# Kernel tuning notes

Hardware: AMD Instinct MI355X
Metric: run time of the kernel (lower is better)

## Reference

```python
import jax, jax.numpy as jnp
import numpy as np

NUM_ITERATIONS = 3


def _squash_elementwise(s):
    # Faithful to the source: squared_norm is summed over the trailing
    # singleton dim, so squash acts elementwise: x^2 * x / ((1+x^2) * |x|).
    sq = s * s
    return sq * s / ((1.0 + sq) * jnp.sqrt(sq))


def setup_inputs() -> dict:
    key = jax.random.key(0)
    k1, k2 = jax.random.split(key)
    B, R, J, O, I = 512, 1152, 10, 16, 8  # batch, num_routes, num_capsules, out_ch, in_ch
    x = jax.random.normal(k1, (B, R, I), dtype=jnp.float32)
    W = jax.random.normal(k2, (R, J, O, I), dtype=jnp.float32)
    return {"x": x, "W": W}


def reference(x, W):
    # u_hat[b,r,j,o] = W[r,j,o,:] @ x[b,r,:]   (the torch matmul over [O,I]x[I,1])
    u_hat = jnp.einsum('rjoi,bri->brjo', W, x)  # [B,R,J,O]
    R, J = W.shape[0], W.shape[1]
    b = jnp.zeros((R, J), dtype=u_hat.dtype)  # b_ij shared across batch
    v = None
    for it in range(NUM_ITERATIONS):
        c = jax.nn.softmax(b, axis=0)                 # softmax over routes (dim=1 in torch)
        s = jnp.einsum('rj,brjo->bjo', c, u_hat)      # weighted sum over routes
        v = _squash_elementwise(s)                    # [B,J,O]
        if it < NUM_ITERATIONS - 1:
            a = jnp.einsum('brjo,bjo->brj', u_hat, v)  # agreement
            b = b + a.mean(axis=0)                     # mean over batch, as in source
    # original returns v_j.squeeze(1) -> [B, num_capsules, out_channels, 1]
    return v[..., None]
```

## Files before the change

kernel.cpp:

```cpp
#include <hip/hip_runtime.h>


#define B_   512
#define R_   1152
#define JO_  160
#define K_   9216

typedef __attribute__((ext_vector_type(4))) float f32x4;
typedef __attribute__((ext_vector_type(8))) short bf16x8;

__device__ __forceinline__ short f2bf(float f) {
  unsigned int u = __float_as_uint(f);
  unsigned int r = (u + 0x7FFFu + ((u >> 16) & 1u)) >> 16;
  return (short)r;
}

__global__ __launch_bounds__(256) void init_kernel(float* __restrict__ bias,
                                                   float* __restrict__ c) {
  int idx = blockIdx.x * 256 + threadIdx.x;
  if (idx < R_ * 10) {
    bias[idx] = 0.0f;
    c[idx] = 1.0f / (float)R_;
  }
}

__global__ __launch_bounds__(256) void xafbuild_kernel(
    const float* __restrict__ x, short* __restrict__ xaf) {
  int gid = blockIdx.x * 256 + threadIdx.x;
  int lane = gid & 63, f = gid >> 6;
  int ks = f % 288, m16 = f / 288;
  int row = m16 * 16 + (lane & 15);
  int k0 = ks * 32 + (lane >> 4) * 8;
  const float4* p = (const float4*)(x + (size_t)row * K_ + k0);
  float4 a = p[0], b = p[1];
  bf16x8 pk;
  pk[0] = f2bf(a.x); pk[1] = f2bf(a.y); pk[2] = f2bf(a.z); pk[3] = f2bf(a.w);
  pk[4] = f2bf(b.x); pk[5] = f2bf(b.y); pk[6] = f2bf(b.z); pk[7] = f2bf(b.w);
  ((bf16x8*)xaf)[gid] = pk;
}

__global__ __launch_bounds__(256) void xtfbuild_kernel(
    const float* __restrict__ x, short* __restrict__ xtf) {
  int gid = blockIdx.x * 256 + threadIdx.x;
  int lane = gid & 63, f = gid >> 6;
  int kb = f & 15, rp = f >> 4;
  int b0 = kb * 32 + (lane >> 4) * 8;
  const float* p = x + (size_t)b0 * K_ + rp * 16 + (lane & 15);
  bf16x8 pk;
#pragma unroll
  for (int t = 0; t < 8; ++t) pk[t] = f2bf(p[(size_t)t * K_]);
  ((bf16x8*)xtf)[gid] = pk;
}

__global__ __launch_bounds__(256) void wcbuild_kernel(
    const float* __restrict__ W, const float* __restrict__ c,
    short* __restrict__ wcf) {
  int idx = blockIdx.x * 256 + threadIdx.x;
  int lane = idx & 63;
  int rest = idx >> 6;
  int nb = rest % 10, kb = rest / 10;
  int k0 = kb * 32 + (lane >> 4) * 8;
  int r = k0 >> 3;
  int j = nb, o = lane & 15;
  const float4* wp = (const float4*)(W + (((size_t)r * 10 + j) * 16 + o) * 8);
  float4 a = wp[0], b = wp[1];
  float cs = c[r * 10 + j];
  bf16x8 pk;
  pk[0] = f2bf(a.x * cs); pk[1] = f2bf(a.y * cs);
  pk[2] = f2bf(a.z * cs); pk[3] = f2bf(a.w * cs);
  pk[4] = f2bf(b.x * cs); pk[5] = f2bf(b.y * cs);
  pk[6] = f2bf(b.z * cs); pk[7] = f2bf(b.w * cs);
  ((bf16x8*)wcf)[idx] = pk;
}

__global__ __launch_bounds__(256) void sgemm_kernel(
    const float* __restrict__ x, const short* __restrict__ xaf,
    const short* __restrict__ wcf, float* __restrict__ part, int spk) {
  const int tid = threadIdx.x;
  const int w = tid >> 6, lane = tid & 63;
  const int m16 = blockIdx.x * 4 + w;
  const int ks0 = blockIdx.y * spk;

  f32x4 acc[10] = {};
  const bf16x8* bp = (const bf16x8*)wcf + ((size_t)ks0 * 640 + lane);
  if (xaf) {
    const bf16x8* ap = (const bf16x8*)xaf + ((size_t)m16 * 288 + ks0) * 64 + lane;
    for (int ks = 0; ks < spk; ++ks) {
      bf16x8 af = ap[0];
      ap += 64;
#pragma unroll
      for (int nb = 0; nb < 10; ++nb)
        acc[nb] = __builtin_amdgcn_mfma_f32_16x16x32_bf16(af, bp[nb * 64],
                                                          acc[nb], 0, 0, 0);
      bp += 640;
    }
  } else {
    const int row = m16 * 16 + (lane & 15);
    const float* xrow = x + (size_t)row * K_ + (lane >> 4) * 8;
    for (int ks = ks0; ks < ks0 + spk; ++ks) {
      const float4* ap = (const float4*)(xrow + ks * 32);
      float4 a0 = ap[0], a1 = ap[1];
      bf16x8 af;
      af[0] = f2bf(a0.x); af[1] = f2bf(a0.y); af[2] = f2bf(a0.z); af[3] = f2bf(a0.w);
      af[4] = f2bf(a1.x); af[5] = f2bf(a1.y); af[6] = f2bf(a1.z); af[7] = f2bf(a1.w);
#pragma unroll
      for (int nb = 0; nb < 10; ++nb)
        acc[nb] = __builtin_amdgcn_mfma_f32_16x16x32_bf16(af, bp[nb * 64],
                                                          acc[nb], 0, 0, 0);
      bp += 640;
    }
  }
  float* pp = part + (size_t)blockIdx.y * (B_ * JO_) +
              (size_t)(m16 * 16 + (lane >> 4) * 4) * JO_ + (lane & 15);
#pragma unroll
  for (int nb = 0; nb < 10; ++nb)
#pragma unroll
    for (int q = 0; q < 4; ++q)
      pp[q * JO_ + nb * 16] = acc[nb][q];
}

template <int KS>
__global__ __launch_bounds__(512) void squash_kernel(
    const float* __restrict__ part, short* __restrict__ vfrag,
    float* __restrict__ out) {
  __shared__ float vsm[32][17];
  const int tid = threadIdx.x;
  const int kb = blockIdx.x / 10, nb = blockIdx.x - (blockIdx.x / 10) * 10;
  const int bl = tid >> 4, col = tid & 15;
  const int b = kb * 32 + bl, jo = nb * 16 + col;
  const float* pe = part + (size_t)b * JO_ + jo;
  float pv[KS];
#pragma unroll
  for (int ks = 0; ks < KS; ++ks) pv[ks] = pe[(size_t)ks * (B_ * JO_)];
  float s = 0.0f;
#pragma unroll
  for (int ks = 0; ks < KS; ++ks) s += pv[ks];
  float val = s * fabsf(s) / (1.0f + s * s);
  if (out) out[(size_t)b * JO_ + jo] = val;
  if (vfrag) {
    vsm[bl][col] = val;
    __syncthreads();
    if (tid < 64) {
      bf16x8 pk;
#pragma unroll
      for (int t = 0; t < 8; ++t)
        pk[t] = f2bf(vsm[(tid >> 4) * 8 + t][tid & 15]);
      ((bf16x8*)vfrag)[(size_t)blockIdx.x * 64 + tid] = pk;
    }
  }
}

__global__ __launch_bounds__(256) void agree_kernel(
    const float* __restrict__ x, const short* __restrict__ xtf,
    const float* __restrict__ W, const short* __restrict__ vfrag,
    float* __restrict__ bias) {
  __shared__ float Msm[4][16][176];
  __shared__ float red[320];
  const int tid = threadIdx.x;
  const int w = tid >> 6, lane = tid & 63;
  const int rp = blockIdx.x;
  const int r0 = rp * 2;

  f32x4 acc[10] = {};
  if (xtf) {
    const bf16x8* ap = (const bf16x8*)xtf + ((size_t)rp * 16 + w * 4) * 64 + lane;
    const bf16x8* bp = (const bf16x8*)vfrag + ((size_t)(w * 4) * 640 + lane);
#pragma unroll
    for (int ks = 0; ks < 4; ++ks) {
      bf16x8 af = ap[0];
      ap += 64;
#pragma unroll
      for (int nb = 0; nb < 10; ++nb)
        acc[nb] = __builtin_amdgcn_mfma_f32_16x16x32_bf16(af, bp[nb * 64],
                                                          acc[nb], 0, 0, 0);
      bp += 640;
    }
  } else {
    const int rowa = lane & 15;
    const float* xp = x + (size_t)rp * 16 + rowa;
    for (int ks = 0; ks < 4; ++ks) {
      int b0 = w * 128 + ks * 32 + (lane >> 4) * 8;
      bf16x8 af;
#pragma unroll
      for (int t = 0; t < 8; ++t) af[t] = f2bf(xp[(size_t)(b0 + t) * K_]);
      const bf16x8* bp = (const bf16x8*)vfrag + ((w * 4 + ks) * 640 + lane);
#pragma unroll
      for (int nb = 0; nb < 10; ++nb)
        acc[nb] = __builtin_amdgcn_mfma_f32_16x16x32_bf16(af, bp[nb * 64],
                                                          acc[nb], 0, 0, 0);
    }
  }
  {
    int colc = lane & 15, rbase = (lane >> 4) * 4;
#pragma unroll
    for (int nb = 0; nb < 10; ++nb)
#pragma unroll
      for (int q = 0; q < 4; ++q)
        Msm[w][rbase + q][nb * 16 + colc] = acc[nb][q];
  }
  __syncthreads();
  for (int idx = tid; idx < 320; idx += 256) {
    int rr = idx / 160, jo = idx - rr * 160;
    int j = jo >> 4, o = jo & 15;
    float p = 0.0f;
    const float* wp = W + (((size_t)(r0 + rr) * 10 + j) * 16 + o) * 8;
#pragma unroll
    for (int i = 0; i < 8; ++i) {
      float m = Msm[0][rr * 8 + i][jo] + Msm[1][rr * 8 + i][jo] +
                Msm[2][rr * 8 + i][jo] + Msm[3][rr * 8 + i][jo];
      p += wp[i] * m;
    }
    red[idx] = p;
  }
  __syncthreads();
  if (tid < 20) {
    int rr = tid / 10, j = tid - rr * 10;
    float s = 0.0f;
#pragma unroll
    for (int o = 0; o < 16; ++o) s += red[rr * 160 + j * 16 + o];
    bias[(r0 + rr) * 10 + j] += s * (1.0f / 512.0f);
  }
}

__global__ __launch_bounds__(256) void softmax_kernel(
    const float* __restrict__ bias, float* __restrict__ c) {
  __shared__ float red[256];
  const int j = blockIdx.x;
  const int tid = threadIdx.x;
  float m = -1e30f;
  for (int r = tid; r < R_; r += 256) m = fmaxf(m, bias[r * 10 + j]);
  red[tid] = m;
  __syncthreads();
  for (int s = 128; s > 0; s >>= 1) {
    if (tid < s) red[tid] = fmaxf(red[tid], red[tid + s]);
    __syncthreads();
  }
  m = red[0];
  __syncthreads();
  float sum = 0.0f;
  for (int r = tid; r < R_; r += 256) sum += expf(bias[r * 10 + j] - m);
  red[tid] = sum;
  __syncthreads();
  for (int s = 128; s > 0; s >>= 1) {
    if (tid < s) red[tid] += red[tid + s];
    __syncthreads();
  }
  float inv = 1.0f / red[0];
  for (int r = tid; r < R_; r += 256)
    c[r * 10 + j] = expf(bias[r * 10 + j] - m) * inv;
}

extern "C" void kernel_launch(void* const* d_in, const int* in_sizes, int n_in,
                              void* d_out, int out_size, void* d_ws,
                              size_t ws_size, hipStream_t stream) {
  const float* x = (const float*)d_in[0];
  const float* W = (const float*)d_in[1];
  float* out = (float*)d_out;
  char* ws = (char*)d_ws;

  const size_t BASE = 3205120;
  const size_t PARTB = 327680;
  const size_t XAFB = 9437184, XTFB = 9437184;

  float* bias  = (float*)(ws);
  float* c     = (float*)(ws + 46080);
  short* wcf   = (short*)(ws + 92160);
  short* vfrag = (short*)(ws + 3041280);

  size_t avail = ws_size > BASE ? ws_size - BASE : 0;
  int KS = 1;
  bool useXaf = false, useXtf = false;
  if (avail >= 32 * PARTB + XAFB + XTFB) { KS = 32; useXaf = useXtf = true; }
  else if (avail >= 16 * PARTB + XAFB + XTFB) { KS = 16; useXaf = useXtf = true; }
  else if (avail >= 16 * PARTB + XAFB) { KS = 16; useXaf = true; }
  else if (avail >= 16 * PARTB) KS = 16;
  else if (avail >= 8 * PARTB) KS = 8;
  else if (avail >= 4 * PARTB) KS = 4;
  else if (avail >= 2 * PARTB) KS = 2;
  int spk = 288 / KS;

  size_t cur = BASE;
  short* xaf = nullptr;
  short* xtf = nullptr;
  if (useXaf) { xaf = (short*)(ws + cur); cur += XAFB; }
  if (useXtf) { xtf = (short*)(ws + cur); cur += XTFB; }
  float* part = (float*)(ws + cur);

  init_kernel<<<45, 256, 0, stream>>>(bias, c);
  if (useXaf) xafbuild_kernel<<<2304, 256, 0, stream>>>(x, xaf);
  if (useXtf) xtfbuild_kernel<<<2304, 256, 0, stream>>>(x, xtf);

  for (int it = 0; it < 3; ++it) {
    wcbuild_kernel<<<720, 256, 0, stream>>>(W, c, wcf);
    sgemm_kernel<<<dim3(8, KS), 256, 0, stream>>>(x, xaf, wcf, part, spk);
    short* vf = (it < 2) ? vfrag : nullptr;
    float* o = (it == 2) ? out : nullptr;
    switch (KS) {
      case 32: squash_kernel<32><<<160, 512, 0, stream>>>(part, vf, o); break;
      case 16: squash_kernel<16><<<160, 512, 0, stream>>>(part, vf, o); break;
      case 8:  squash_kernel<8><<<160, 512, 0, stream>>>(part, vf, o); break;
      case 4:  squash_kernel<4><<<160, 512, 0, stream>>>(part, vf, o); break;
      case 2:  squash_kernel<2><<<160, 512, 0, stream>>>(part, vf, o); break;
      default: squash_kernel<1><<<160, 512, 0, stream>>>(part, vf, o); break;
    }
    if (it < 2) {
      agree_kernel<<<576, 256, 0, stream>>>(x, xtf, W, vfrag, bias);
      softmax_kernel<<<10, 256, 0, stream>>>(bias, c);
    }
  }
}
```

Baseline: 98.31 us.

## Fuse split-K GEMM with squash via in-block LDS reduction

Replaces the split-K sgemm plus separate squash kernel with a single forward kernel that splits K across four wave groups inside one block and reduces their partials through shared memory before applying squash. This removes the global partial buffer and one launch per iteration. The first iteration applies the uniform 1/1152 coupling as a scalar instead of scaling W. The cost is far less parallelism: only 16 blocks each run a 72-step MFMA loop, where before the grid was 8 by up to 32 blocks.

```diff
diff --git a/kernel.cpp b/kernel.cpp
--- a/kernel.cpp
+++ b/kernel.cpp
@@ -15,13 +15,9 @@
   return (short)r;
 }
 
-__global__ __launch_bounds__(256) void init_kernel(float* __restrict__ bias,
-                                                   float* __restrict__ c) {
+__global__ __launch_bounds__(256) void init_kernel(float* __restrict__ bias) {
   int idx = blockIdx.x * 256 + threadIdx.x;
-  if (idx < R_ * 10) {
-    bias[idx] = 0.0f;
-    c[idx] = 1.0f / (float)R_;
-  }
+  if (idx < R_ * 10) bias[idx] = 0.0f;
 }
 
 __global__ __launch_bounds__(256) void xafbuild_kernel(
@@ -64,7 +60,7 @@
   int j = nb, o = lane & 15;
   const float4* wp = (const float4*)(W + (((size_t)r * 10 + j) * 16 + o) * 8);
   float4 a = wp[0], b = wp[1];
-  float cs = c[r * 10 + j];
+  float cs = c ? c[r * 10 + j] : 1.0f;
   bf16x8 pk;
   pk[0] = f2bf(a.x * cs); pk[1] = f2bf(a.y * cs);
   pk[2] = f2bf(a.z * cs); pk[3] = f2bf(a.w * cs);
@@ -73,19 +69,24 @@
   ((bf16x8*)wcf)[idx] = pk;
 }
 
-__global__ __launch_bounds__(256) void sgemm_kernel(
+template <bool SCALE>
+__global__ __launch_bounds__(512) void fwd_kernel(
     const float* __restrict__ x, const short* __restrict__ xaf,
-    const short* __restrict__ wcf, float* __restrict__ part, int spk) {
+    const short* __restrict__ wcf, short* __restrict__ vfrag,
+    float* __restrict__ out) {
+  __shared__ float sm[20992];
   const int tid = threadIdx.x;
   const int w = tid >> 6, lane = tid & 63;
-  const int m16 = blockIdx.x * 4 + w;
-  const int ks0 = blockIdx.y * spk;
+  const int mw = w & 1, kw = w >> 1;
+  const int bb = blockIdx.x;
+  const int m16 = bb * 2 + mw;
 
   f32x4 acc[10] = {};
-  const bf16x8* bp = (const bf16x8*)wcf + ((size_t)ks0 * 640 + lane);
+  const bf16x8* bp = (const bf16x8*)wcf + ((size_t)(kw * 72) * 640 + lane);
   if (xaf) {
-    const bf16x8* ap = (const bf16x8*)xaf + ((size_t)m16 * 288 + ks0) * 64 + lane;
-    for (int ks = 0; ks < spk; ++ks) {
+    const bf16x8* ap =
+        (const bf16x8*)xaf + ((size_t)m16 * 288 + kw * 72) * 64 + lane;
+    for (int st = 0; st < 72; ++st) {
       bf16x8 af = ap[0];
       ap += 64;
 #pragma unroll
@@ -95,14 +96,16 @@
       bp += 640;
     }
   } else {
-    const int row = m16 * 16 + (lane & 15);
+    const int row = bb * 32 + mw * 16 + (lane & 15);
     const float* xrow = x + (size_t)row * K_ + (lane >> 4) * 8;
-    for (int ks = ks0; ks < ks0 + spk; ++ks) {
-      const float4* ap = (const float4*)(xrow + ks * 32);
-      float4 a0 = ap[0], a1 = ap[1];
+    for (int st = 0; st < 72; ++st) {
+      const float4* apf = (const float4*)(xrow + (kw * 72 + st) * 32);
+      float4 a0 = apf[0], a1 = apf[1];
       bf16x8 af;
-      af[0] = f2bf(a0.x); af[1] = f2bf(a0.y); af[2] = f2bf(a0.z); af[3] = f2bf(a0.w);
-      af[4] = f2bf(a1.x); af[5] = f2bf(a1.y); af[6] = f2bf(a1.z); af[7] = f2bf(a1.w);
+      af[0] = f2bf(a0.x); af[1] = f2bf(a0.y);
+      af[2] = f2bf(a0.z); af[3] = f2bf(a0.w);
+      af[4] = f2bf(a1.x); af[5] = f2bf(a1.y);
+      af[6] = f2bf(a1.z); af[7] = f2bf(a1.w);
 #pragma unroll
       for (int nb = 0; nb < 10; ++nb)
         acc[nb] = __builtin_amdgcn_mfma_f32_16x16x32_bf16(af, bp[nb * 64],
@@ -110,42 +113,57 @@
       bp += 640;
     }
   }
-  float* pp = part + (size_t)blockIdx.y * (B_ * JO_) +
-              (size_t)(m16 * 16 + (lane >> 4) * 4) * JO_ + (lane & 15);
-#pragma unroll
-  for (int nb = 0; nb < 10; ++nb)
-#pragma unroll
-    for (int q = 0; q < 4; ++q)
-      pp[q * JO_ + nb * 16] = acc[nb][q];
-}
-
-template <int KS>
-__global__ __launch_bounds__(512) void squash_kernel(
-    const float* __restrict__ part, short* __restrict__ vfrag,
-    float* __restrict__ out) {
-  __shared__ float vsm[32][17];
-  const int tid = threadIdx.x;
-  const int kb = blockIdx.x / 10, nb = blockIdx.x - (blockIdx.x / 10) * 10;
-  const int bl = tid >> 4, col = tid & 15;
-  const int b = kb * 32 + bl, jo = nb * 16 + col;
-  const float* pe = part + (size_t)b * JO_ + jo;
-  float pv[KS];
-#pragma unroll
-  for (int ks = 0; ks < KS; ++ks) pv[ks] = pe[(size_t)ks * (B_ * JO_)];
-  float s = 0.0f;
-#pragma unroll
-  for (int ks = 0; ks < KS; ++ks) s += pv[ks];
-  float val = s * fabsf(s) / (1.0f + s * s);
-  if (out) out[(size_t)b * JO_ + jo] = val;
+  {
+    float* dst = sm + (size_t)(w * 64 + lane) * 41;
+#pragma unroll
+    for (int nb = 0; nb < 10; ++nb)
+#pragma unroll
+      for (int q = 0; q < 4; ++q) dst[nb * 4 + q] = acc[nb][q];
+  }
+  __syncthreads();
+  float vals[10];
+  const int e0 = tid * 10;
+  const int mwr = e0 / 2560;
+  const int rem = e0 - mwr * 2560;
+  const int lr = rem / 40, c0 = rem - lr * 40;
+#pragma unroll
+  for (int u = 0; u < 10; ++u) {
+    int cc = c0 + u;
+    float s = sm[((0 + mwr) * 64 + lr) * 41 + cc] +
+              sm[((2 + mwr) * 64 + lr) * 41 + cc] +
+              sm[((4 + mwr) * 64 + lr) * 41 + cc] +
+              sm[((6 + mwr) * 64 + lr) * 41 + cc];
+    if (SCALE) s *= (1.0f / 1152.0f);
+    vals[u] = s * fabsf(s) / (1.0f + s * s);
+  }
+  if (out) {
+#pragma unroll
+    for (int u = 0; u < 10; ++u) {
+      int cc = c0 + u;
+      int q = cc & 3, nb = cc >> 2;
+      int bl = mwr * 16 + (lr >> 4) * 4 + q;
+      int jo = nb * 16 + (lr & 15);
+      out[(size_t)(bb * 32 + bl) * JO_ + jo] = vals[u];
+    }
+  }
   if (vfrag) {
-    vsm[bl][col] = val;
     __syncthreads();
-    if (tid < 64) {
+#pragma unroll
+    for (int u = 0; u < 10; ++u) {
+      int cc = c0 + u;
+      int q = cc & 3, nb = cc >> 2;
+      int bl = mwr * 16 + (lr >> 4) * 4 + q;
+      int jo = nb * 16 + (lr & 15);
+      sm[bl * 162 + jo] = vals[u];
+    }
+    __syncthreads();
+    for (int ch = tid; ch < 640; ch += 512) {
+      int nb = ch >> 6, l2 = ch & 63;
       bf16x8 pk;
 #pragma unroll
       for (int t = 0; t < 8; ++t)
-        pk[t] = f2bf(vsm[(tid >> 4) * 8 + t][tid & 15]);
-      ((bf16x8*)vfrag)[(size_t)blockIdx.x * 64 + tid] = pk;
+        pk[t] = f2bf(sm[((l2 >> 4) * 8 + t) * 162 + nb * 16 + (l2 & 15)]);
+      ((bf16x8*)vfrag)[(size_t)(bb * 10 + nb) * 64 + l2] = pk;
     }
   }
 }
@@ -259,7 +277,6 @@
   char* ws = (char*)d_ws;
 
   const size_t BASE = 3205120;
-  const size_t PARTB = 327680;
   const size_t XAFB = 9437184, XTFB = 9437184;
 
   float* bias  = (float*)(ws);
@@ -267,42 +284,24 @@
   short* wcf   = (short*)(ws + 92160);
   short* vfrag = (short*)(ws + 3041280);
 
-  size_t avail = ws_size > BASE ? ws_size - BASE : 0;
-  int KS = 1;
-  bool useXaf = false, useXtf = false;
-  if (avail >= 32 * PARTB + XAFB + XTFB) { KS = 32; useXaf = useXtf = true; }
-  else if (avail >= 16 * PARTB + XAFB + XTFB) { KS = 16; useXaf = useXtf = true; }
-  else if (avail >= 16 * PARTB + XAFB) { KS = 16; useXaf = true; }
-  else if (avail >= 16 * PARTB) KS = 16;
-  else if (avail >= 8 * PARTB) KS = 8;
-  else if (avail >= 4 * PARTB) KS = 4;
-  else if (avail >= 2 * PARTB) KS = 2;
-  int spk = 288 / KS;
-
-  size_t cur = BASE;
   short* xaf = nullptr;
   short* xtf = nullptr;
-  if (useXaf) { xaf = (short*)(ws + cur); cur += XAFB; }
-  if (useXtf) { xtf = (short*)(ws + cur); cur += XTFB; }
-  float* part = (float*)(ws + cur);
-
-  init_kernel<<<45, 256, 0, stream>>>(bias, c);
-  if (useXaf) xafbuild_kernel<<<2304, 256, 0, stream>>>(x, xaf);
-  if (useXtf) xtfbuild_kernel<<<2304, 256, 0, stream>>>(x, xtf);
+  size_t cur = BASE;
+  if (ws_size >= cur + XAFB) { xaf = (short*)(ws + cur); cur += XAFB; }
+  if (ws_size >= cur + XTFB) { xtf = (short*)(ws + cur); cur += XTFB; }
+
+  init_kernel<<<45, 256, 0, stream>>>(bias);
+  if (xaf) xafbuild_kernel<<<2304, 256, 0, stream>>>(x, xaf);
+  if (xtf) xtfbuild_kernel<<<2304, 256, 0, stream>>>(x, xtf);
 
   for (int it = 0; it < 3; ++it) {
-    wcbuild_kernel<<<720, 256, 0, stream>>>(W, c, wcf);
-    sgemm_kernel<<<dim3(8, KS), 256, 0, stream>>>(x, xaf, wcf, part, spk);
+    wcbuild_kernel<<<720, 256, 0, stream>>>(W, (it == 0) ? nullptr : c, wcf);
     short* vf = (it < 2) ? vfrag : nullptr;
     float* o = (it == 2) ? out : nullptr;
-    switch (KS) {
-      case 32: squash_kernel<32><<<160, 512, 0, stream>>>(part, vf, o); break;
-      case 16: squash_kernel<16><<<160, 512, 0, stream>>>(part, vf, o); break;
-      case 8:  squash_kernel<8><<<160, 512, 0, stream>>>(part, vf, o); break;
-      case 4:  squash_kernel<4><<<160, 512, 0, stream>>>(part, vf, o); break;
-      case 2:  squash_kernel<2><<<160, 512, 0, stream>>>(part, vf, o); break;
-      default: squash_kernel<1><<<160, 512, 0, stream>>>(part, vf, o); break;
-    }
+    if (it == 0)
+      fwd_kernel<true><<<16, 512, 0, stream>>>(x, xaf, wcf, vf, o);
+    else
+      fwd_kernel<false><<<16, 512, 0, stream>>>(x, xaf, wcf, vf, o);
     if (it < 2) {
       agree_kernel<<<576, 256, 0, stream>>>(x, xtf, W, vfrag, bias);
       softmax_kernel<<<10, 256, 0, stream>>>(bias, c);
```

Result: slower. 367.4 us (+273.8%).

## Fuse coupling-weight construction into sgemm via LDS and drop init/softmax passes

Applied to the files above, without the earlier changes.

Removes the separate wcbuild and softmax kernels. Each sgemm block now builds its bf16 W*c tile directly in shared memory, computing c from bias plus per-capsule max and inverse-sum produced by a small stat kernel. The first iteration uses a uniform scale applied at the epilogue, and bias zeroing is folded into xafbuild. The workspace-dependent fallback paths are dropped, so the kernel now assumes a large workspace with KS fixed at 32. Each block recomputes 5760 W fragments and exps into 92KB of LDS, which may limit occupancy and duplicates W reads across the 8 x-blocks.

```diff
diff --git a/kernel.cpp b/kernel.cpp
--- a/kernel.cpp
+++ b/kernel.cpp
@@ -5,6 +5,8 @@
 #define R_   1152
 #define JO_  160
 #define K_   9216
+#define KS_  32
+#define SPK_ 9
 
 typedef __attribute__((ext_vector_type(4))) float f32x4;
 typedef __attribute__((ext_vector_type(8))) short bf16x8;
@@ -15,18 +17,11 @@
   return (short)r;
 }
 
-__global__ __launch_bounds__(256) void init_kernel(float* __restrict__ bias,
-                                                   float* __restrict__ c) {
-  int idx = blockIdx.x * 256 + threadIdx.x;
-  if (idx < R_ * 10) {
-    bias[idx] = 0.0f;
-    c[idx] = 1.0f / (float)R_;
-  }
-}
-
 __global__ __launch_bounds__(256) void xafbuild_kernel(
-    const float* __restrict__ x, short* __restrict__ xaf) {
+    const float* __restrict__ x, short* __restrict__ xaf,
+    float* __restrict__ bias) {
   int gid = blockIdx.x * 256 + threadIdx.x;
+  if (gid < R_ * 10) bias[gid] = 0.0f;
   int lane = gid & 63, f = gid >> 6;
   int ks = f % 288, m16 = f / 288;
   int row = m16 * 16 + (lane & 15);
@@ -52,74 +47,91 @@
   ((bf16x8*)xtf)[gid] = pk;
 }
 
-__global__ __launch_bounds__(256) void wcbuild_kernel(
-    const float* __restrict__ W, const float* __restrict__ c,
-    short* __restrict__ wcf) {
-  int idx = blockIdx.x * 256 + threadIdx.x;
-  int lane = idx & 63;
-  int rest = idx >> 6;
-  int nb = rest % 10, kb = rest / 10;
-  int k0 = kb * 32 + (lane >> 4) * 8;
-  int r = k0 >> 3;
-  int j = nb, o = lane & 15;
-  const float4* wp = (const float4*)(W + (((size_t)r * 10 + j) * 16 + o) * 8);
-  float4 a = wp[0], b = wp[1];
-  float cs = c[r * 10 + j];
-  bf16x8 pk;
-  pk[0] = f2bf(a.x * cs); pk[1] = f2bf(a.y * cs);
-  pk[2] = f2bf(a.z * cs); pk[3] = f2bf(a.w * cs);
-  pk[4] = f2bf(b.x * cs); pk[5] = f2bf(b.y * cs);
-  pk[6] = f2bf(b.z * cs); pk[7] = f2bf(b.w * cs);
-  ((bf16x8*)wcf)[idx] = pk;
-}
-
+__global__ __launch_bounds__(256) void stat_kernel(
+    const float* __restrict__ bias, float* __restrict__ mz) {
+  __shared__ float red[256];
+  const int j = blockIdx.x;
+  const int tid = threadIdx.x;
+  float m = -1e30f;
+  for (int r = tid; r < R_; r += 256) m = fmaxf(m, bias[r * 10 + j]);
+  red[tid] = m;
+  __syncthreads();
+  for (int s = 128; s > 0; s >>= 1) {
+    if (tid < s) red[tid] = fmaxf(red[tid], red[tid + s]);
+    __syncthreads();
+  }
+  m = red[0];
+  __syncthreads();
+  float sum = 0.0f;
+  for (int r = tid; r < R_; r += 256) sum += expf(bias[r * 10 + j] - m);
+  red[tid] = sum;
+  __syncthreads();
+  for (int s = 128; s > 0; s >>= 1) {
+    if (tid < s) red[tid] += red[tid + s];
+    __syncthreads();
+  }
+  if (tid == 0) {
+    mz[j] = m;
+    mz[10 + j] = 1.0f / red[0];
+  }
+}
+
+template <bool NEEDC>
 __global__ __launch_bounds__(256) void sgemm_kernel(
-    const float* __restrict__ x, const short* __restrict__ xaf,
-    const short* __restrict__ wcf, float* __restrict__ part, int spk) {
+    const short* __restrict__ xaf, const float* __restrict__ W,
+    const float* __restrict__ bias, const float* __restrict__ mz,
+    float* __restrict__ part) {
+  __shared__ short wls[5760 * 8];
   const int tid = threadIdx.x;
   const int w = tid >> 6, lane = tid & 63;
+  const int ks0 = blockIdx.y * SPK_;
+  bf16x8* wls8 = (bf16x8*)wls;
+
+  for (int q = 0; q < 23; ++q) {
+    int idx = q * 256 + tid;
+    if (idx < 5760) {
+      int l = idx & 63, sn = idx >> 6;
+      int nb = sn % 10, st = sn / 10;
+      int r = (ks0 + st) * 4 + (l >> 4);
+      int o = l & 15;
+      const float4* wp =
+          (const float4*)(W + (((size_t)r * 10 + nb) * 16 + o) * 8);
+      float4 a = wp[0], b = wp[1];
+      float cs = 1.0f;
+      if (NEEDC) cs = expf(bias[r * 10 + nb] - mz[nb]) * mz[10 + nb];
+      bf16x8 pk;
+      pk[0] = f2bf(a.x * cs); pk[1] = f2bf(a.y * cs);
+      pk[2] = f2bf(a.z * cs); pk[3] = f2bf(a.w * cs);
+      pk[4] = f2bf(b.x * cs); pk[5] = f2bf(b.y * cs);
+      pk[6] = f2bf(b.z * cs); pk[7] = f2bf(b.w * cs);
+      wls8[idx] = pk;
+    }
+  }
+  __syncthreads();
+
   const int m16 = blockIdx.x * 4 + w;
-  const int ks0 = blockIdx.y * spk;
-
   f32x4 acc[10] = {};
-  const bf16x8* bp = (const bf16x8*)wcf + ((size_t)ks0 * 640 + lane);
-  if (xaf) {
-    const bf16x8* ap = (const bf16x8*)xaf + ((size_t)m16 * 288 + ks0) * 64 + lane;
-    for (int ks = 0; ks < spk; ++ks) {
-      bf16x8 af = ap[0];
-      ap += 64;
-#pragma unroll
-      for (int nb = 0; nb < 10; ++nb)
-        acc[nb] = __builtin_amdgcn_mfma_f32_16x16x32_bf16(af, bp[nb * 64],
-                                                          acc[nb], 0, 0, 0);
-      bp += 640;
-    }
-  } else {
-    const int row = m16 * 16 + (lane & 15);
-    const float* xrow = x + (size_t)row * K_ + (lane >> 4) * 8;
-    for (int ks = ks0; ks < ks0 + spk; ++ks) {
-      const float4* ap = (const float4*)(xrow + ks * 32);
-      float4 a0 = ap[0], a1 = ap[1];
-      bf16x8 af;
-      af[0] = f2bf(a0.x); af[1] = f2bf(a0.y); af[2] = f2bf(a0.z); af[3] = f2bf(a0.w);
-      af[4] = f2bf(a1.x); af[5] = f2bf(a1.y); af[6] = f2bf(a1.z); af[7] = f2bf(a1.w);
-#pragma unroll
-      for (int nb = 0; nb < 10; ++nb)
-        acc[nb] = __builtin_amdgcn_mfma_f32_16x16x32_bf16(af, bp[nb * 64],
-                                                          acc[nb], 0, 0, 0);
-      bp += 640;
-    }
-  }
+  const bf16x8* ap = (const bf16x8*)xaf + ((size_t)m16 * 288 + ks0) * 64 + lane;
+  const bf16x8* lp = wls8 + lane;
+  for (int st = 0; st < SPK_; ++st) {
+    bf16x8 af = ap[0];
+    ap += 64;
+#pragma unroll
+    for (int nb = 0; nb < 10; ++nb)
+      acc[nb] = __builtin_amdgcn_mfma_f32_16x16x32_bf16(af, lp[nb * 64],
+                                                        acc[nb], 0, 0, 0);
+    lp += 640;
+  }
+  const float scale = NEEDC ? 1.0f : (1.0f / 1152.0f);
   float* pp = part + (size_t)blockIdx.y * (B_ * JO_) +
               (size_t)(m16 * 16 + (lane >> 4) * 4) * JO_ + (lane & 15);
 #pragma unroll
   for (int nb = 0; nb < 10; ++nb)
 #pragma unroll
     for (int q = 0; q < 4; ++q)
-      pp[q * JO_ + nb * 16] = acc[nb][q];
-}
-
-template <int KS>
+      pp[q * JO_ + nb * 16] = acc[nb][q] * scale;
+}
+
 __global__ __launch_bounds__(512) void squash_kernel(
     const float* __restrict__ part, short* __restrict__ vfrag,
     float* __restrict__ out) {
@@ -129,12 +141,12 @@
   const int bl = tid >> 4, col = tid & 15;
   const int b = kb * 32 + bl, jo = nb * 16 + col;
   const float* pe = part + (size_t)b * JO_ + jo;
-  float pv[KS];
-#pragma unroll
-  for (int ks = 0; ks < KS; ++ks) pv[ks] = pe[(size_t)ks * (B_ * JO_)];
+  float pv[KS_];
+#pragma unroll
+  for (int ks = 0; ks < KS_; ++ks) pv[ks] = pe[(size_t)ks * (B_ * JO_)];
   float s = 0.0f;
 #pragma unroll
-  for (int ks = 0; ks < KS; ++ks) s += pv[ks];
+  for (int ks = 0; ks < KS_; ++ks) s += pv[ks];
   float val = s * fabsf(s) / (1.0f + s * s);
   if (out) out[(size_t)b * JO_ + jo] = val;
   if (vfrag) {
@@ -151,9 +163,8 @@
 }
 
 __global__ __launch_bounds__(256) void agree_kernel(
-    const float* __restrict__ x, const short* __restrict__ xtf,
-    const float* __restrict__ W, const short* __restrict__ vfrag,
-    float* __restrict__ bias) {
+    const short* __restrict__ xtf, const float* __restrict__ W,
+    const short* __restrict__ vfrag, float* __restrict__ bias) {
   __shared__ float Msm[4][16][176];
   __shared__ float red[320];
   const int tid = threadIdx.x;
@@ -162,33 +173,17 @@
   const int r0 = rp * 2;
 
   f32x4 acc[10] = {};
-  if (xtf) {
-    const bf16x8* ap = (const bf16x8*)xtf + ((size_t)rp * 16 + w * 4) * 64 + lane;
-    const bf16x8* bp = (const bf16x8*)vfrag + ((size_t)(w * 4) * 640 + lane);
-#pragma unroll
-    for (int ks = 0; ks < 4; ++ks) {
-      bf16x8 af = ap[0];
-      ap += 64;
-#pragma unroll
-      for (int nb = 0; nb < 10; ++nb)
-        acc[nb] = __builtin_amdgcn_mfma_f32_16x16x32_bf16(af, bp[nb * 64],
-                                                          acc[nb], 0, 0, 0);
-      bp += 640;
-    }
-  } else {
-    const int rowa = lane & 15;
-    const float* xp = x + (size_t)rp * 16 + rowa;
-    for (int ks = 0; ks < 4; ++ks) {
-      int b0 = w * 128 + ks * 32 + (lane >> 4) * 8;
-      bf16x8 af;
-#pragma unroll
-      for (int t = 0; t < 8; ++t) af[t] = f2bf(xp[(size_t)(b0 + t) * K_]);
-      const bf16x8* bp = (const bf16x8*)vfrag + ((w * 4 + ks) * 640 + lane);
-#pragma unroll
-      for (int nb = 0; nb < 10; ++nb)
-        acc[nb] = __builtin_amdgcn_mfma_f32_16x16x32_bf16(af, bp[nb * 64],
-                                                          acc[nb], 0, 0, 0);
-    }
+  const bf16x8* ap = (const bf16x8*)xtf + ((size_t)rp * 16 + w * 4) * 64 + lane;
+  const bf16x8* bp = (const bf16x8*)vfrag + ((size_t)(w * 4) * 640 + lane);
+#pragma unroll
+  for (int ks = 0; ks < 4; ++ks) {
+    bf16x8 af = ap[0];
+    ap += 64;
+#pragma unroll
+    for (int nb = 0; nb < 10; ++nb)
+      acc[nb] = __builtin_amdgcn_mfma_f32_16x16x32_bf16(af, bp[nb * 64],
+                                                        acc[nb], 0, 0, 0);
+    bp += 640;
   }
   {
     int colc = lane & 15, rbase = (lane >> 4) * 4;
@@ -220,34 +215,6 @@
     for (int o = 0; o < 16; ++o) s += red[rr * 160 + j * 16 + o];
     bias[(r0 + rr) * 10 + j] += s * (1.0f / 512.0f);
   }
-}
-
-__global__ __launch_bounds__(256) void softmax_kernel(
-    const float* __restrict__ bias, float* __restrict__ c) {
-  __shared__ float red[256];
-  const int j = blockIdx.x;
-  const int tid = threadIdx.x;
-  float m = -1e30f;
-  for (int r = tid; r < R_; r += 256) m = fmaxf(m, bias[r * 10 + j]);
-  red[tid] = m;
-  __syncthreads();
-  for (int s = 128; s > 0; s >>= 1) {
-    if (tid < s) red[tid] = fmaxf(red[tid], red[tid + s]);
-    __syncthreads();
-  }
-  m = red[0];
-  __syncthreads();
-  float sum = 0.0f;
-  for (int r = tid; r < R_; r += 256) sum += expf(bias[r * 10 + j] - m);
-  red[tid] = sum;
-  __syncthreads();
-  for (int s = 128; s > 0; s >>= 1) {
-    if (tid < s) red[tid] += red[tid + s];
-    __syncthreads();
-  }
-  float inv = 1.0f / red[0];
-  for (int r = tid; r < R_; r += 256)
-    c[r * 10 + j] = expf(bias[r * 10 + j] - m) * inv;
 }
 
 extern "C" void kernel_launch(void* const* d_in, const int* in_sizes, int n_in,
@@ -258,54 +225,25 @@
   float* out = (float*)d_out;
   char* ws = (char*)d_ws;
 
-  const size_t BASE = 3205120;
-  const size_t PARTB = 327680;
-  const size_t XAFB = 9437184, XTFB = 9437184;
-
   float* bias  = (float*)(ws);
-  float* c     = (float*)(ws + 46080);
-  short* wcf   = (short*)(ws + 92160);
-  short* vfrag = (short*)(ws + 3041280);
-
-  size_t avail = ws_size > BASE ? ws_size - BASE : 0;
-  int KS = 1;
-  bool useXaf = false, useXtf = false;
-  if (avail >= 32 * PARTB + XAFB + XTFB) { KS = 32; useXaf = useXtf = true; }
-  else if (avail >= 16 * PARTB + XAFB + XTFB) { KS = 16; useXaf = useXtf = true; }
-  else if (avail >= 16 * PARTB + XAFB) { KS = 16; useXaf = true; }
-  else if (avail >= 16 * PARTB) KS = 16;
-  else if (avail >= 8 * PARTB) KS = 8;
-  else if (avail >= 4 * PARTB) KS = 4;
-  else if (avail >= 2 * PARTB) KS = 2;
-  int spk = 288 / KS;
-
-  size_t cur = BASE;
-  short* xaf = nullptr;
-  short* xtf = nullptr;
-  if (useXaf) { xaf = (short*)(ws + cur); cur += XAFB; }
-  if (useXtf) { xtf = (short*)(ws + cur); cur += XTFB; }
-  float* part = (float*)(ws + cur);
-
-  init_kernel<<<45, 256, 0, stream>>>(bias, c);
-  if (useXaf) xafbuild_kernel<<<2304, 256, 0, stream>>>(x, xaf);
-  if (useXtf) xtfbuild_kernel<<<2304, 256, 0, stream>>>(x, xtf);
-
-  for (int it = 0; it < 3; ++it) {
-    wcbuild_kernel<<<720, 256, 0, stream>>>(W, c, wcf);
-    sgemm_kernel<<<dim3(8, KS), 256, 0, stream>>>(x, xaf, wcf, part, spk);
-    short* vf = (it < 2) ? vfrag : nullptr;
-    float* o = (it == 2) ? out : nullptr;
-    switch (KS) {
-      case 32: squash_kernel<32><<<160, 512, 0, stream>>>(part, vf, o); break;
-      case 16: squash_kernel<16><<<160, 512, 0, stream>>>(part, vf, o); break;
-      case 8:  squash_kernel<8><<<160, 512, 0, stream>>>(part, vf, o); break;
-      case 4:  squash_kernel<4><<<160, 512, 0, stream>>>(part, vf, o); break;
-      case 2:  squash_kernel<2><<<160, 512, 0, stream>>>(part, vf, o); break;
-      default: squash_kernel<1><<<160, 512, 0, stream>>>(part, vf, o); break;
-    }
-    if (it < 2) {
-      agree_kernel<<<576, 256, 0, stream>>>(x, xtf, W, vfrag, bias);
-      softmax_kernel<<<10, 256, 0, stream>>>(bias, c);
-    }
-  }
-}
+  float* mz    = (float*)(ws + 46080);
+  short* vfrag = (short*)(ws + 46160);
+  short* xaf   = (short*)(ws + 210000);
+  short* xtf   = (short*)(ws + 9647184);
+  float* part  = (float*)(ws + 19084368);
+
+  xafbuild_kernel<<<2304, 256, 0, stream>>>(x, xaf, bias);
+  xtfbuild_kernel<<<2304, 256, 0, stream>>>(x, xtf);
+
+  sgemm_kernel<false><<<dim3(8, KS_), 256, 0, stream>>>(xaf, W, nullptr,
+                                                        nullptr, part);
+  squash_kernel<<<160, 512, 0, stream>>>(part, vfrag, nullptr);
+  agree_kernel<<<576, 256, 0, stream>>>(xtf, W, vfrag, bias);
+  stat_kernel<<<10, 256, 0, stream>>>(bias, mz);
+  sgemm_kernel<true><<<dim3(8, KS_), 256, 0, stream>>>(xaf, W, bias, mz, part);
+  squash_kernel<<<160, 512, 0, stream>>>(part, vfrag, nullptr);
+  agree_kernel<<<576, 256, 0, stream>>>(xtf, W, vfrag, bias);
+  stat_kernel<<<10, 256, 0, stream>>>(bias, mz);
+  sgemm_kernel<true><<<dim3(8, KS_), 256, 0, stream>>>(xaf, W, bias, mz, part);
+  squash_kernel<<<160, 512, 0, stream>>>(part, nullptr, out);
+}
```

After: 113.2 us. 1.15x slower.
